# Optimization experiments

Hardware: AMD Instinct MI355X
Metric: run time of the kernel (lower is better)

Reference implementation:

```python
import jax, jax.numpy as jnp
import numpy as np

IN_CH = 128
N_HEAD = 16
D_K = 4
D_MODEL = 256
T_PE = 1000.0
EPS = 1e-5


def setup_inputs() -> dict:
    key = jax.random.key(0)
    ks = jax.random.split(key, 8)
    sz_b, L, h, w = 4, 30, 64, 64
    x = jax.random.normal(ks[0], (sz_b, L, IN_CH, h, w), dtype=jnp.float32)
    batch_positions = jnp.sort(jax.random.randint(ks[1], (sz_b, L), 0, 365), axis=1).astype(jnp.int32)
    pad_mask = jnp.zeros((sz_b, L), dtype=bool)
    gn_weight = jnp.ones((IN_CH,), dtype=jnp.float32)
    gn_bias = jnp.zeros((IN_CH,), dtype=jnp.float32)
    conv_w = jax.random.normal(ks[2], (D_MODEL, IN_CH), dtype=jnp.float32) * (1.0 / np.sqrt(IN_CH))
    conv_b = jnp.zeros((D_MODEL,), dtype=jnp.float32)
    Q = jax.random.normal(ks[3], (N_HEAD, D_K), dtype=jnp.float32) * np.sqrt(2.0 / D_K)
    Wk = jax.random.normal(ks[4], (N_HEAD * D_K, D_MODEL), dtype=jnp.float32) * np.sqrt(2.0 / D_K)
    bk = jnp.zeros((N_HEAD * D_K,), dtype=jnp.float32)
    return {"x": x, "gn_weight": gn_weight, "gn_bias": gn_bias,
            "conv_w": conv_w, "conv_b": conv_b, "Q": Q, "Wk": Wk, "bk": bk,
            "batch_positions": batch_positions, "pad_mask": pad_mask}


def reference(x, gn_weight, gn_bias, conv_w, conv_b, Q, Wk, bk, batch_positions, pad_mask):
    n_head, d_k = Q.shape
    sz_b, L, d, h, w = x.shape
    B = sz_b * h * w
    # flatten pixels: [B, L, C]
    out = x.transpose(0, 3, 4, 1, 2).reshape(B, L, d)
    # GroupNorm(num_groups=n_head) over channels and time per pixel-sample
    g = out.transpose(0, 2, 1).reshape(B, n_head, d // n_head, L)
    mu = g.mean(axis=(2, 3), keepdims=True)
    var = g.var(axis=(2, 3), keepdims=True)
    g = (g - mu) / jnp.sqrt(var + EPS)
    out = g.reshape(B, d, L) * gn_weight[None, :, None] + gn_bias[None, :, None]
    out = out.transpose(0, 2, 1)  # [B, L, C]
    # 1x1 Conv1d == per-timestep linear projection to d_model
    out = out @ conv_w.T + conv_b  # [B, L, d_model]
    d_model = conv_w.shape[0]
    # sinusoidal positional encoding on dates, repeated over heads
    d_pe = d_model // n_head
    idx = jnp.arange(d_pe)
    denom = jnp.power(jnp.float32(T_PE), 2.0 * (idx // 2).astype(jnp.float32) / d_pe)
    tab = batch_positions.astype(jnp.float32)[:, :, None] / denom  # [sz_b, L, d_pe]
    pe = jnp.where(idx % 2 == 0, jnp.sin(tab), jnp.cos(tab))
    pe = jnp.tile(pe, (1, 1, n_head))  # [sz_b, L, d_model]
    out = (out.reshape(sz_b, h * w, L, d_model) + pe[:, None, :, :]).reshape(B, L, d_model)
    # keys and learned-query attention scores, temperature = sqrt(d_k)
    k = (out @ Wk.T + bk).reshape(B, L, n_head, d_k)
    scores = jnp.einsum('hd,blhd->hbl', Q, k) / jnp.sqrt(jnp.float32(d_k))
    scores = scores.reshape(n_head, sz_b, h * w, L)
    scores = jnp.where(pad_mask[None, :, None, :], jnp.float32(-1000.0), scores)
    attn = jax.nn.softmax(scores, axis=-1)
    # [n_head, sz_b, L, h, w]
    return attn.reshape(n_head, sz_b, h, w, L).transpose(0, 1, 4, 2, 3)
```

## Files before the change

kernel.cpp:

```cpp
#include <hip/hip_runtime.h>


#define EPSV 1e-5f

#define WS_U    0
#define WS_UU   2048
#define WS_P2   2304
#define WS_FLAG 4224
#define WS_QT   4352
#define WS_WT   8448
#define WS_INV  10496
#define WS_MUI  272640

__global__ void __launch_bounds__(1024) k0(const float* __restrict__ Q,
                                           const float* __restrict__ Wk,
                                           const float* __restrict__ conv_w,
                                           const float* __restrict__ gn_w,
                                           const float* __restrict__ conv_b,
                                           const float* __restrict__ gn_b,
                                           const float* __restrict__ bk,
                                           const int* __restrict__ bpos,
                                           const unsigned char* __restrict__ pmask,
                                           float* __restrict__ ws) {
    int t = threadIdx.x;
    for (int i = t; i < 4096; i += 1024) {
        int h = i >> 8, m = i & 255;
        float s = 0.f;
        #pragma unroll
        for (int d = 0; d < 4; ++d) s += Q[h*4+d] * Wk[(h*4+d)*256 + m];
        ws[WS_QT + h*256 + m] = s;
    }
    __syncthreads();
    for (int i = t; i < 2048; i += 1024) {
        int h = i >> 7, c = i & 127;
        const float* qt = ws + WS_QT + h*256;
        float s = 0.f;
        #pragma unroll 8
        for (int m = 0; m < 256; ++m) s += qt[m] * conv_w[m*128 + c];
        ws[WS_WT + h*128 + c] = s;
        ws[WS_U  + c*16  + h] = s * gn_w[c];
    }
    __syncthreads();
    __shared__ float sc[16];
    __shared__ float qsv[256];
    __shared__ float rden[16];
    if (t < 256) {
        int h = t >> 4, g = t & 15;
        float s = 0.f;
        #pragma unroll
        for (int cc = 0; cc < 8; ++cc) s += ws[WS_U + (g*8+cc)*16 + h];
        ws[WS_UU + g*16 + h] = s;
        float q = 0.f;
        #pragma unroll
        for (int r = 0; r < 16; ++r) q += ws[WS_QT + h*256 + r*16 + g];
        qsv[h*16 + g] = q;
    }
    if (t < 16) {
        int h = t;
        float wb = 0.f;
        for (int c = 0; c < 128; ++c) wb += ws[WS_WT + h*128 + c] * gn_b[c];
        float s0 = 0.f;
        for (int m = 0; m < 256; ++m) s0 += ws[WS_QT + h*256 + m] * conv_b[m];
        #pragma unroll
        for (int d = 0; d < 4; ++d) s0 += Q[h*4+d] * bk[h*4+d];
        sc[h] = wb + s0;
        rden[t] = powf(1000.0f, -((float)(t >> 1)) * 0.125f);
    }
    if (t < 120) ws[WS_FLAG + t] = pmask[t] ? 1.f : 0.f;
    __syncthreads();
    for (int idx = t; idx < 1920; idx += 1024) {
        int h = idx / 120, r = idx - h*120;
        float pos = (float)bpos[r];
        float pt = 0.f;
        #pragma unroll
        for (int p = 0; p < 16; ++p) {
            float tab = pos * rden[p];
            float v = (p & 1) ? cosf(tab) : sinf(tab);
            pt += v * qsv[h*16 + p];
        }
        ws[WS_P2 + r*16 + h] = pt + sc[h];
    }
}

__global__ void __launch_bounds__(256) k1(const float* __restrict__ x,
                                          float* __restrict__ ws) {
    int bx = blockIdx.x;
    int g = bx >> 5;
    int pq = (bx & 31)*256 + threadIdx.x;
    int pix0 = pq*2;
    int b = pix0 >> 12, pij = pix0 & 4095;
    const float2* xp = (const float2*)(x + (b*30*128 + g*8)*4096 + pij);
    float sx = 0.f, sy = 0.f, ssx = 0.f, ssy = 0.f;
    for (int l = 0; l < 30; ++l) {
        const float2* xl = xp + l*128*2048;
        #pragma unroll
        for (int c = 0; c < 8; ++c) {
            float2 v = xl[c*2048];
            sx += v.x; sy += v.y;
            ssx += v.x*v.x; ssy += v.y*v.y;
        }
    }
    float mux = sx*(1.f/240.f), muy = sy*(1.f/240.f);
    float ivx = rsqrtf(ssx*(1.f/240.f) - mux*mux + EPSV);
    float ivy = rsqrtf(ssy*(1.f/240.f) - muy*muy + EPSV);
    *(float2*)(ws + WS_INV + g*16384 + pix0) = make_float2(ivx, ivy);
    *(float2*)(ws + WS_MUI + g*16384 + pix0) = make_float2(mux*ivx, muy*ivy);
}

#define FMA4(A, S, V) { (A).x += (S)*(V).x; (A).y += (S)*(V).y; (A).z += (S)*(V).z; (A).w += (S)*(V).w; }
#define NMA4(A, S, V) { (A).x -= (S)*(V).x; (A).y -= (S)*(V).y; (A).z -= (S)*(V).z; (A).w -= (S)*(V).w; }

__global__ void __launch_bounds__(256) k2(const float* __restrict__ x,
                                          const float* __restrict__ ws,
                                          float* __restrict__ out) {
    __shared__ float su[2048];
    __shared__ float sU[256];
    __shared__ float sP2[16];
    __shared__ float sflag;
    int t = threadIdx.x;
    int bx = blockIdx.x;
    int pb2 = bx / 30, l = bx - pb2*30;
    int pixbase = pb2 * 1024;
    int b = pixbase >> 12;
    int pijb = pixbase & 4095;
    int bl = b*30 + l;
    int pij = pijb + t*4;
    int pix0 = pixbase + t*4;

    for (int i = t; i < 512; i += 256)
        *(float4*)(su + i*4) = *(const float4*)(ws + WS_U + i*4);
    sU[t] = ws[WS_UU + t];
    if (t < 16) sP2[t] = ws[WS_P2 + bl*16 + t];
    if (t == 0) sflag = ws[WS_FLAG + bl];
    __syncthreads();

    float4 acc[16];
    #pragma unroll
    for (int h = 0; h < 16; ++h) acc[h] = make_float4(0.f, 0.f, 0.f, 0.f);
    const float* xbase = x + (bl*128)*4096 + pij;
    #pragma unroll 1
    for (int g = 0; g < 16; ++g) {
        float4 inv = *(const float4*)(ws + WS_INV + g*16384 + pix0);
        float4 mui = *(const float4*)(ws + WS_MUI + g*16384 + pix0);
        const float* us = su + g*128;
        #pragma unroll
        for (int q = 0; q < 4; ++q) {
            float4 Ug = *(const float4*)(sU + g*16 + q*4);
            NMA4(acc[q*4+0], Ug.x, mui); NMA4(acc[q*4+1], Ug.y, mui);
            NMA4(acc[q*4+2], Ug.z, mui); NMA4(acc[q*4+3], Ug.w, mui);
        }
        const float* xg = xbase + g*8*4096;
        #pragma unroll
        for (int cc = 0; cc < 8; ++cc) {
            float4 v = *(const float4*)(xg + cc*4096);
            float4 xs;
            xs.x = v.x*inv.x; xs.y = v.y*inv.y; xs.z = v.z*inv.z; xs.w = v.w*inv.w;
            #pragma unroll
            for (int q = 0; q < 4; ++q) {
                float4 uq = *(const float4*)(us + cc*16 + q*4);
                FMA4(acc[q*4+0], uq.x, xs); FMA4(acc[q*4+1], uq.y, xs);
                FMA4(acc[q*4+2], uq.z, xs); FMA4(acc[q*4+3], uq.w, xs);
            }
        }
    }
    bool msk = (sflag != 0.f);
    #pragma unroll
    for (int h = 0; h < 16; ++h) {
        float p2 = sP2[h];
        float4 sv;
        sv.x = 0.5f*(acc[h].x + p2); sv.y = 0.5f*(acc[h].y + p2);
        sv.z = 0.5f*(acc[h].z + p2); sv.w = 0.5f*(acc[h].w + p2);
        if (msk) sv = make_float4(-1000.f, -1000.f, -1000.f, -1000.f);
        *(float4*)(out + ((h*4 + b)*30 + l)*4096 + pij) = sv;
    }
}

__global__ void __launch_bounds__(256) k3(float* __restrict__ out) {
    int idx = blockIdx.x*256 + threadIdx.x;
    int hb = idx >> 10;
    int pij = (idx & 1023)*4;
    float* p = out + hb*30*4096 + pij;
    float4 v[30];
    float4 m = make_float4(-1e30f, -1e30f, -1e30f, -1e30f);
    #pragma unroll
    for (int l = 0; l < 30; ++l) {
        v[l] = *(const float4*)(p + l*4096);
        m.x = fmaxf(m.x, v[l].x); m.y = fmaxf(m.y, v[l].y);
        m.z = fmaxf(m.z, v[l].z); m.w = fmaxf(m.w, v[l].w);
    }
    float4 s = make_float4(0.f, 0.f, 0.f, 0.f);
    #pragma unroll
    for (int l = 0; l < 30; ++l) {
        v[l].x = __expf(v[l].x - m.x); s.x += v[l].x;
        v[l].y = __expf(v[l].y - m.y); s.y += v[l].y;
        v[l].z = __expf(v[l].z - m.z); s.z += v[l].z;
        v[l].w = __expf(v[l].w - m.w); s.w += v[l].w;
    }
    float4 r; r.x = 1.f/s.x; r.y = 1.f/s.y; r.z = 1.f/s.z; r.w = 1.f/s.w;
    #pragma unroll
    for (int l = 0; l < 30; ++l) {
        float4 o;
        o.x = v[l].x*r.x; o.y = v[l].y*r.y; o.z = v[l].z*r.z; o.w = v[l].w*r.w;
        *(float4*)(p + l*4096) = o;
    }
}

extern "C" void kernel_launch(void* const* d_in, const int* in_sizes, int n_in,
                              void* d_out, int out_size, void* d_ws, size_t ws_size,
                              hipStream_t stream) {
    const float* x      = (const float*)d_in[0];
    const float* gn_w   = (const float*)d_in[1];
    const float* gn_b   = (const float*)d_in[2];
    const float* conv_w = (const float*)d_in[3];
    const float* conv_b = (const float*)d_in[4];
    const float* Q      = (const float*)d_in[5];
    const float* Wk     = (const float*)d_in[6];
    const float* bk     = (const float*)d_in[7];
    const int*   bpos   = (const int*)d_in[8];
    const unsigned char* pmask = (const unsigned char*)d_in[9];
    float* ws  = (float*)d_ws;
    float* out = (float*)d_out;

    hipLaunchKernelGGL(k0, dim3(1),   dim3(1024), 0, stream,
                       Q, Wk, conv_w, gn_w, conv_b, gn_b, bk, bpos, pmask, ws);
    hipLaunchKernelGGL(k1, dim3(512), dim3(256),  0, stream, x, ws);
    hipLaunchKernelGGL(k2, dim3(480), dim3(256),  0, stream, x, ws, out);
    hipLaunchKernelGGL(k3, dim3(256), dim3(256),  0, stream, out);
}
```

Baseline: 156.0 us.

## Merge weight-precompute kernel into stats kernel and halve softmax per-thread width

Folds the single-block weight/positional precompute kernel into the GroupNorm statistics kernel as an extra block, so both run concurrently and one launch is removed. The softmax kernel now processes two pixels per thread with twice as many blocks to raise parallelism, and the main projection loop is unrolled by two. The precompute block now has 256 threads instead of 1024, so it may become a longer serial tail running alongside the stats blocks.

```diff
diff --git a/kernel.cpp b/kernel.cpp
--- a/kernel.cpp
+++ b/kernel.cpp
@@ -12,7 +12,7 @@
 #define WS_INV  10496
 #define WS_MUI  272640
 
-__global__ void __launch_bounds__(1024) k0(const float* __restrict__ Q,
+__global__ void __launch_bounds__(256) k01(const float* __restrict__ Q,
                                            const float* __restrict__ Wk,
                                            const float* __restrict__ conv_w,
                                            const float* __restrict__ gn_w,
@@ -21,72 +21,74 @@
                                            const float* __restrict__ bk,
                                            const int* __restrict__ bpos,
                                            const unsigned char* __restrict__ pmask,
+                                           const float* __restrict__ x,
                                            float* __restrict__ ws) {
-    int t = threadIdx.x;
-    for (int i = t; i < 4096; i += 1024) {
-        int h = i >> 8, m = i & 255;
-        float s = 0.f;
-        #pragma unroll
-        for (int d = 0; d < 4; ++d) s += Q[h*4+d] * Wk[(h*4+d)*256 + m];
-        ws[WS_QT + h*256 + m] = s;
-    }
-    __syncthreads();
-    for (int i = t; i < 2048; i += 1024) {
-        int h = i >> 7, c = i & 127;
-        const float* qt = ws + WS_QT + h*256;
-        float s = 0.f;
-        #pragma unroll 8
-        for (int m = 0; m < 256; ++m) s += qt[m] * conv_w[m*128 + c];
-        ws[WS_WT + h*128 + c] = s;
-        ws[WS_U  + c*16  + h] = s * gn_w[c];
-    }
-    __syncthreads();
     __shared__ float sc[16];
     __shared__ float qsv[256];
     __shared__ float rden[16];
-    if (t < 256) {
-        int h = t >> 4, g = t & 15;
-        float s = 0.f;
-        #pragma unroll
-        for (int cc = 0; cc < 8; ++cc) s += ws[WS_U + (g*8+cc)*16 + h];
-        ws[WS_UU + g*16 + h] = s;
-        float q = 0.f;
-        #pragma unroll
-        for (int r = 0; r < 16; ++r) q += ws[WS_QT + h*256 + r*16 + g];
-        qsv[h*16 + g] = q;
-    }
-    if (t < 16) {
-        int h = t;
-        float wb = 0.f;
-        for (int c = 0; c < 128; ++c) wb += ws[WS_WT + h*128 + c] * gn_b[c];
-        float s0 = 0.f;
-        for (int m = 0; m < 256; ++m) s0 += ws[WS_QT + h*256 + m] * conv_b[m];
-        #pragma unroll
-        for (int d = 0; d < 4; ++d) s0 += Q[h*4+d] * bk[h*4+d];
-        sc[h] = wb + s0;
-        rden[t] = powf(1000.0f, -((float)(t >> 1)) * 0.125f);
-    }
-    if (t < 120) ws[WS_FLAG + t] = pmask[t] ? 1.f : 0.f;
-    __syncthreads();
-    for (int idx = t; idx < 1920; idx += 1024) {
-        int h = idx / 120, r = idx - h*120;
-        float pos = (float)bpos[r];
-        float pt = 0.f;
-        #pragma unroll
-        for (int p = 0; p < 16; ++p) {
-            float tab = pos * rden[p];
-            float v = (p & 1) ? cosf(tab) : sinf(tab);
-            pt += v * qsv[h*16 + p];
-        }
-        ws[WS_P2 + r*16 + h] = pt + sc[h];
-    }
-}
-
-__global__ void __launch_bounds__(256) k1(const float* __restrict__ x,
-                                          float* __restrict__ ws) {
+    int t = threadIdx.x;
     int bx = blockIdx.x;
+    if (bx == 512) {
+        for (int i = t; i < 4096; i += 256) {
+            int h = i >> 8, m = i & 255;
+            float s = 0.f;
+            #pragma unroll
+            for (int d = 0; d < 4; ++d) s += Q[h*4+d] * Wk[(h*4+d)*256 + m];
+            ws[WS_QT + h*256 + m] = s;
+        }
+        __syncthreads();
+        for (int i = t; i < 2048; i += 256) {
+            int h = i >> 7, c = i & 127;
+            const float* qt = ws + WS_QT + h*256;
+            float s = 0.f;
+            #pragma unroll 32
+            for (int m = 0; m < 256; ++m) s += qt[m] * conv_w[m*128 + c];
+            ws[WS_WT + h*128 + c] = s;
+            ws[WS_U  + c*16  + h] = s * gn_w[c];
+        }
+        __syncthreads();
+        {
+            int h = t >> 4, g = t & 15;
+            float s = 0.f;
+            #pragma unroll
+            for (int cc = 0; cc < 8; ++cc) s += ws[WS_U + (g*8+cc)*16 + h];
+            ws[WS_UU + g*16 + h] = s;
+            float q = 0.f;
+            #pragma unroll
+            for (int r = 0; r < 16; ++r) q += ws[WS_QT + h*256 + r*16 + g];
+            qsv[h*16 + g] = q;
+        }
+        if (t < 16) {
+            int h = t;
+            float wb = 0.f;
+            #pragma unroll 16
+            for (int c = 0; c < 128; ++c) wb += ws[WS_WT + h*128 + c] * gn_b[c];
+            float s0 = 0.f;
+            #pragma unroll 16
+            for (int m = 0; m < 256; ++m) s0 += ws[WS_QT + h*256 + m] * conv_b[m];
+            #pragma unroll
+            for (int d = 0; d < 4; ++d) s0 += Q[h*4+d] * bk[h*4+d];
+            sc[h] = wb + s0;
+            rden[t] = powf(1000.0f, -((float)(t >> 1)) * 0.125f);
+        }
+        if (t < 120) ws[WS_FLAG + t] = pmask[t] ? 1.f : 0.f;
+        __syncthreads();
+        for (int idx = t; idx < 1920; idx += 256) {
+            int h = idx / 120, r = idx - h*120;
+            float pos = (float)bpos[r];
+            float pt = 0.f;
+            #pragma unroll
+            for (int p = 0; p < 16; ++p) {
+                float tab = pos * rden[p];
+                float v = (p & 1) ? cosf(tab) : sinf(tab);
+                pt += v * qsv[h*16 + p];
+            }
+            ws[WS_P2 + r*16 + h] = pt + sc[h];
+        }
+        return;
+    }
     int g = bx >> 5;
-    int pq = (bx & 31)*256 + threadIdx.x;
+    int pq = (bx & 31)*256 + t;
     int pix0 = pq*2;
     int b = pix0 >> 12, pij = pix0 & 4095;
     const float2* xp = (const float2*)(x + (b*30*128 + g*8)*4096 + pij);
@@ -138,7 +140,7 @@
     #pragma unroll
     for (int h = 0; h < 16; ++h) acc[h] = make_float4(0.f, 0.f, 0.f, 0.f);
     const float* xbase = x + (bl*128)*4096 + pij;
-    #pragma unroll 1
+    #pragma unroll 2
     for (int g = 0; g < 16; ++g) {
         float4 inv = *(const float4*)(ws + WS_INV + g*16384 + pix0);
         float4 mui = *(const float4*)(ws + WS_MUI + g*16384 + pix0);
@@ -177,31 +179,26 @@
 
 __global__ void __launch_bounds__(256) k3(float* __restrict__ out) {
     int idx = blockIdx.x*256 + threadIdx.x;
-    int hb = idx >> 10;
-    int pij = (idx & 1023)*4;
+    int hb = idx >> 11;
+    int pij = (idx & 2047)*2;
     float* p = out + hb*30*4096 + pij;
-    float4 v[30];
-    float4 m = make_float4(-1e30f, -1e30f, -1e30f, -1e30f);
-    #pragma unroll
-    for (int l = 0; l < 30; ++l) {
-        v[l] = *(const float4*)(p + l*4096);
-        m.x = fmaxf(m.x, v[l].x); m.y = fmaxf(m.y, v[l].y);
-        m.z = fmaxf(m.z, v[l].z); m.w = fmaxf(m.w, v[l].w);
-    }
-    float4 s = make_float4(0.f, 0.f, 0.f, 0.f);
-    #pragma unroll
-    for (int l = 0; l < 30; ++l) {
-        v[l].x = __expf(v[l].x - m.x); s.x += v[l].x;
-        v[l].y = __expf(v[l].y - m.y); s.y += v[l].y;
-        v[l].z = __expf(v[l].z - m.z); s.z += v[l].z;
-        v[l].w = __expf(v[l].w - m.w); s.w += v[l].w;
-    }
-    float4 r; r.x = 1.f/s.x; r.y = 1.f/s.y; r.z = 1.f/s.z; r.w = 1.f/s.w;
-    #pragma unroll
-    for (int l = 0; l < 30; ++l) {
-        float4 o;
-        o.x = v[l].x*r.x; o.y = v[l].y*r.y; o.z = v[l].z*r.z; o.w = v[l].w*r.w;
-        *(float4*)(p + l*4096) = o;
+    float2 v[30];
+    float m0 = -1e30f, m1 = -1e30f;
+    #pragma unroll
+    for (int l = 0; l < 30; ++l) {
+        v[l] = *(const float2*)(p + l*4096);
+        m0 = fmaxf(m0, v[l].x); m1 = fmaxf(m1, v[l].y);
+    }
+    float s0 = 0.f, s1 = 0.f;
+    #pragma unroll
+    for (int l = 0; l < 30; ++l) {
+        v[l].x = __expf(v[l].x - m0); s0 += v[l].x;
+        v[l].y = __expf(v[l].y - m1); s1 += v[l].y;
+    }
+    float r0 = 1.f/s0, r1 = 1.f/s1;
+    #pragma unroll
+    for (int l = 0; l < 30; ++l) {
+        *(float2*)(p + l*4096) = make_float2(v[l].x*r0, v[l].y*r1);
     }
 }
 
@@ -221,9 +218,8 @@
     float* ws  = (float*)d_ws;
     float* out = (float*)d_out;
 
-    hipLaunchKernelGGL(k0, dim3(1),   dim3(1024), 0, stream,
-                       Q, Wk, conv_w, gn_w, conv_b, gn_b, bk, bpos, pmask, ws);
-    hipLaunchKernelGGL(k1, dim3(512), dim3(256),  0, stream, x, ws);
-    hipLaunchKernelGGL(k2, dim3(480), dim3(256),  0, stream, x, ws, out);
-    hipLaunchKernelGGL(k3, dim3(256), dim3(256),  0, stream, out);
-}
+    hipLaunchKernelGGL(k01, dim3(513), dim3(256), 0, stream,
+                       Q, Wk, conv_w, gn_w, conv_b, gn_b, bk, bpos, pmask, x, ws);
+    hipLaunchKernelGGL(k2,  dim3(480), dim3(256), 0, stream, x, ws, out);
+    hipLaunchKernelGGL(k3,  dim3(512), dim3(256), 0, stream, out);
+}
```

Result: slower. 165.5 us (+6.1%).
